# Kernel optimization log

Measured on AMD Instinct MI355X. Metric: run time of the kernel, lower is better.

Reference implementation:

```python
import jax, jax.numpy as jnp
import numpy as np

NUM_TERMS = 8
NUM_CHANNELS = 64
BATCH = 8
NODES = 2048


def setup_inputs() -> dict:
    key = jax.random.key(0)
    kA, kh = jax.random.split(key)
    A = jax.random.normal(kA, (BATCH, NODES, NODES), dtype=jnp.float32)
    # xavier_uniform over (num_terms+1, num_channels)
    fan_in, fan_out = NUM_TERMS + 1, NUM_CHANNELS
    limit = float(np.sqrt(6.0 / (fan_in + fan_out)))
    h = jax.random.uniform(kh, (NUM_TERMS + 1, NUM_CHANNELS), dtype=jnp.float32,
                           minval=-limit, maxval=limit)
    return {"A": A, "h": h}


def reference(A, h):
    # Y[b,n,c] = h[0,c] + sum_{i=1..T} h[i,c] * diag(A^i)[b,n]
    num_terms = h.shape[0] - 1
    diags = []  # each [B, N]: diagonal of A^i
    Ap = A
    for i in range(num_terms):
        if i > 0:
            Ap = jnp.matmul(Ap, A)  # A^(i+1), computed once per power
        diags.append(jnp.diagonal(Ap, axis1=-2, axis2=-1))
    D = jnp.stack(diags, axis=0)  # [T, B, N]
    # fuse per-channel weighted sum of diagonals into one einsum
    out = jnp.einsum("tbn,tc->bnc", D, h[1:])
    out = out + h[0][None, None, :]  # identity term: diag(I) == 1
    return out
```

## Files before the change

### kernel.cpp

```cpp
#include <hip/hip_runtime.h>
#include <hip/hip_bf16.h>

#define NN 2048
#define BB 8
#define NC 64

typedef __bf16 bf16_8 __attribute__((ext_vector_type(8)));
typedef __bf16 bf16_4 __attribute__((ext_vector_type(4)));
typedef float f32x16 __attribute__((ext_vector_type(16)));

__device__ __forceinline__ void gll16(const void* g, void* l) {
  __builtin_amdgcn_global_load_lds((const __attribute__((address_space(1))) void*)g,
                                   (__attribute__((address_space(3))) void*)l,
                                   16, 0, 0);
}

__global__ __launch_bounds__(256)
void k_convert(const float* __restrict__ A, __bf16* __restrict__ Ab, __bf16* __restrict__ At) {
  __shared__ __bf16 tile[64][65];
  int b = blockIdx.z;
  const float* Asrc = A + (size_t)b * NN * NN;
  __bf16* Abd = Ab + (size_t)b * NN * NN;
  __bf16* Atd = At + (size_t)b * NN * NN;
  int r0 = blockIdx.y * 64, c0 = blockIdx.x * 64;
  int row = threadIdx.x >> 4;
  int col4 = (threadIdx.x & 15) * 4;
#pragma unroll
  for (int rr = 0; rr < 64; rr += 16) {
    float4 v = *(const float4*)&Asrc[(size_t)(r0 + row + rr) * NN + c0 + col4];
    bf16_4 hv;
    hv[0] = (__bf16)v.x; hv[1] = (__bf16)v.y; hv[2] = (__bf16)v.z; hv[3] = (__bf16)v.w;
    *(bf16_4*)&Abd[(size_t)(r0 + row + rr) * NN + c0 + col4] = hv;
    tile[row + rr][col4 + 0] = hv[0];
    tile[row + rr][col4 + 1] = hv[1];
    tile[row + rr][col4 + 2] = hv[2];
    tile[row + rr][col4 + 3] = hv[3];
  }
  __syncthreads();
  int row2 = threadIdx.x >> 3;
  int col8 = (threadIdx.x & 7) * 8;
#pragma unroll
  for (int rr = 0; rr < 64; rr += 32) {
    bf16_8 v;
#pragma unroll
    for (int j = 0; j < 8; ++j) v[j] = tile[col8 + j][row2 + rr];
    *(bf16_8*)&Atd[(size_t)(c0 + row2 + rr) * NN + r0 + col8] = v;
  }
}

__global__ __launch_bounds__(256, 2)
void k_gemm_bt(const __bf16* __restrict__ P, const __bf16* __restrict__ Q,
               __bf16* __restrict__ C, __bf16* __restrict__ Ct) {
  __shared__ __align__(16) __bf16 smem[24576];
  __bf16 (*As)[64] = (__bf16(*)[64])smem;
  __bf16 (*Bs)[64] = (__bf16(*)[64])(smem + 16384);
  int b = blockIdx.z;
  const __bf16* Pb = P + (size_t)b * NN * NN;
  const __bf16* Qb = Q + (size_t)b * NN * NN;
  __bf16* Cb = C + (size_t)b * NN * NN;
  int tid = threadIdx.x;
  int wave = tid >> 6;
  int lane = tid & 63;
  int tm = blockIdx.y * 256;
  int tn = blockIdx.x * 128;
  int wm = (wave >> 1) * 128;
  int wn = (wave & 1) * 64;

  int srow = lane >> 3;
  int sc = (lane & 7) ^ srow;
  int arowA = wave * 64;
  int arowB = wave * 32;
  const __bf16* pA = Pb + (size_t)(tm + arowA + srow) * NN + sc * 8;
  const __bf16* pB = Qb + (size_t)(tn + arowB + srow) * NN + sc * 8;

  int am = lane & 31;
  int ah = lane >> 5;

  f32x16 acc[4][2] = {};

  for (int k0 = 0; k0 < NN; k0 += 64) {
#pragma unroll
    for (int g = 0; g < 8; ++g)
      gll16(pA + (size_t)(g * 8) * NN + k0, &As[arowA + g * 8][0]);
#pragma unroll
    for (int g = 0; g < 4; ++g)
      gll16(pB + (size_t)(g * 8) * NN + k0, &Bs[arowB + g * 8][0]);
    __syncthreads();
#pragma unroll
    for (int ks = 0; ks < 4; ++ks) {
      int cch = ks * 2 + ah;
      bf16_8 af[4], bf2[2];
#pragma unroll
      for (int i = 0; i < 4; ++i) {
        int ra = wm + i * 32 + am;
        af[i] = *(const bf16_8*)&As[ra][(cch ^ (ra & 7)) * 8];
      }
#pragma unroll
      for (int i = 0; i < 2; ++i) {
        int rb2 = wn + i * 32 + am;
        bf2[i] = *(const bf16_8*)&Bs[rb2][(cch ^ (rb2 & 7)) * 8];
      }
#pragma unroll
      for (int im = 0; im < 4; ++im)
#pragma unroll
        for (int in = 0; in < 2; ++in)
          acc[im][in] = __builtin_amdgcn_mfma_f32_32x32x16_bf16(af[im], bf2[in], acc[im][in], 0, 0, 0);
    }
    __syncthreads();
  }

  int cc = lane & 31;
  int rq = (lane >> 5) * 4;
#pragma unroll
  for (int im = 0; im < 4; ++im)
#pragma unroll
    for (int in = 0; in < 2; ++in)
#pragma unroll
      for (int reg = 0; reg < 16; ++reg) {
        int row = (reg & 3) + 8 * (reg >> 2) + rq;
        Cb[(size_t)(tm + wm + im * 32 + row) * NN + (tn + wn + in * 32 + cc)] =
            (__bf16)acc[im][in][reg];
      }

  if (Ct != nullptr) {
    __bf16* Ctb = Ct + (size_t)b * NN * NN;
    __bf16 (*Tt)[258] = (__bf16(*)[258])smem;
#pragma unroll
    for (int ch = 0; ch < 2; ++ch) {
      __syncthreads();
      if ((wave & 1) == ch) {
#pragma unroll
        for (int im = 0; im < 4; ++im)
#pragma unroll
          for (int in = 0; in < 2; ++in)
#pragma unroll
            for (int g = 0; g < 4; ++g) {
              bf16_4 v;
#pragma unroll
              for (int r = 0; r < 4; ++r) v[r] = (__bf16)acc[im][in][g * 4 + r];
              *(bf16_4*)&Tt[in * 32 + cc][wm + im * 32 + rq + 8 * g] = v;
            }
      }
      __syncthreads();
#pragma unroll
      for (int p = 0; p < 4; ++p) {
        int trow = p * 16 + (tid >> 4);
        int tcol = (tid & 15) * 16;
        bf16_8 v0 = *(const bf16_8*)&Tt[trow][tcol];
        bf16_8 v1 = *(const bf16_8*)&Tt[trow][tcol + 8];
        size_t gr = (size_t)(tn + ch * 64 + trow) * NN + tm + tcol;
        *(bf16_8*)&Ctb[gr] = v0;
        *(bf16_8*)&Ctb[gr + 8] = v1;
      }
    }
  }
}

__global__ __launch_bounds__(256)
void k_reduce(const float* __restrict__ A, const float* __restrict__ h,
              const __bf16* __restrict__ At, const __bf16* __restrict__ A2,
              const __bf16* __restrict__ A2t, const __bf16* __restrict__ A3t,
              const __bf16* __restrict__ A4, const __bf16* __restrict__ A4t,
              float* __restrict__ out) {
  int b = blockIdx.y;
  int wave = threadIdx.x >> 6, lane = threadIdx.x & 63;
  int n = blockIdx.x * 4 + wave;
  size_t mb = (size_t)b * NN * NN;
  size_t rb = mb + (size_t)n * NN;
  float d5 = 0, d6 = 0, d7 = 0, d8 = 0;
  for (int c = 0; c < NN; c += 512) {
    int k = c + lane * 8;
    bf16_8 va4  = *(const bf16_8*)(A4 + rb + k);
    bf16_8 vat  = *(const bf16_8*)(At + rb + k);
    bf16_8 va2t = *(const bf16_8*)(A2t + rb + k);
    bf16_8 va3t = *(const bf16_8*)(A3t + rb + k);
    bf16_8 va4t = *(const bf16_8*)(A4t + rb + k);
#pragma unroll
    for (int j = 0; j < 8; ++j) {
      float f4 = (float)va4[j];
      d5 += f4 * (float)vat[j];
      d6 += f4 * (float)va2t[j];
      d7 += f4 * (float)va3t[j];
      d8 += f4 * (float)va4t[j];
    }
  }
#pragma unroll
  for (int off = 32; off > 0; off >>= 1) {
    d5 += __shfl_xor(d5, off);
    d6 += __shfl_xor(d6, off);
    d7 += __shfl_xor(d7, off);
    d8 += __shfl_xor(d8, off);
  }
  float d1 = A[mb + (size_t)n * NN + n];
  float d2 = (float)A2[rb + n];
  float d3 = (float)A3t[rb + n];
  float d4 = (float)A4[rb + n];
  float r = h[lane] + h[64 + lane] * d1 + h[128 + lane] * d2 + h[192 + lane] * d3 +
            h[256 + lane] * d4 + h[320 + lane] * d5 + h[384 + lane] * d6 +
            h[448 + lane] * d7 + h[512 + lane] * d8;
  out[((size_t)b * NN + n) * NC + lane] = r;
}

extern "C" void kernel_launch(void* const* d_in, const int* in_sizes, int n_in,
                              void* d_out, int out_size, void* d_ws, size_t ws_size,
                              hipStream_t stream) {
  const float* A = (const float*)d_in[0];
  const float* h = (const float*)d_in[1];
  float* out = (float*)d_out;

  size_t elems = (size_t)BB * NN * NN;
  __bf16* Ab  = (__bf16*)d_ws;
  __bf16* At  = Ab + elems;
  __bf16* A2  = At + elems;
  __bf16* A2t = A2 + elems;
  __bf16* A3t = A2t + elems;
  __bf16* A4  = A3t + elems;
  __bf16* A4t = Ab;

  dim3 bl(256);
  k_convert<<<dim3(32, 32, BB), bl, 0, stream>>>(A, Ab, At);
  k_gemm_bt<<<dim3(16, 8, BB), bl, 0, stream>>>(Ab, At, A2, A2t);
  k_gemm_bt<<<dim3(16, 8, BB), bl, 0, stream>>>(At, A2, A3t, nullptr);
  k_gemm_bt<<<dim3(16, 8, BB), bl, 0, stream>>>(A2, A2t, A4, A4t);
  k_reduce<<<dim3(NN / 4, BB), bl, 0, stream>>>(A, h, At, A2, A2t, A3t, A4, A4t, out);
}
```

Before: 724.9 us.

## Merge the two independent power GEMMs into one launch and raise occupancy

The GEMM body becomes a device function. The A^3 and A^4 products, which depend only on A^2, now run as two jobs selected by blockIdx.z inside a single launch. This removes one kernel boundary and lets the blocks of both GEMMs fill the device together, which should cut tail idle time. Launch bounds go from 2 to 3 blocks per CU to allow more resident blocks, at the risk of register pressure or spills for the 128-float accumulator.

```diff
diff --git a/kernel.cpp b/kernel.cpp
--- a/kernel.cpp
+++ b/kernel.cpp
@@ -48,21 +48,17 @@
   }
 }
 
-__global__ __launch_bounds__(256, 2)
-void k_gemm_bt(const __bf16* __restrict__ P, const __bf16* __restrict__ Q,
-               __bf16* __restrict__ C, __bf16* __restrict__ Ct) {
-  __shared__ __align__(16) __bf16 smem[24576];
+__device__ __forceinline__
+void gemm_body(const __bf16* __restrict__ Pb, const __bf16* __restrict__ Qb,
+               __bf16* __restrict__ Cb, __bf16* __restrict__ Ctb,
+               __bf16* smem, int tmBlk, int tnBlk) {
   __bf16 (*As)[64] = (__bf16(*)[64])smem;
   __bf16 (*Bs)[64] = (__bf16(*)[64])(smem + 16384);
-  int b = blockIdx.z;
-  const __bf16* Pb = P + (size_t)b * NN * NN;
-  const __bf16* Qb = Q + (size_t)b * NN * NN;
-  __bf16* Cb = C + (size_t)b * NN * NN;
   int tid = threadIdx.x;
   int wave = tid >> 6;
   int lane = tid & 63;
-  int tm = blockIdx.y * 256;
-  int tn = blockIdx.x * 128;
+  int tm = tmBlk * 256;
+  int tn = tnBlk * 128;
   int wm = (wave >> 1) * 128;
   int wn = (wave & 1) * 64;
 
@@ -122,8 +118,7 @@
             (__bf16)acc[im][in][reg];
       }
 
-  if (Ct != nullptr) {
-    __bf16* Ctb = Ct + (size_t)b * NN * NN;
+  if (Ctb != nullptr) {
     __bf16 (*Tt)[258] = (__bf16(*)[258])smem;
 #pragma unroll
     for (int ch = 0; ch < 2; ++ch) {
@@ -154,6 +149,28 @@
       }
     }
   }
+}
+
+__global__ __launch_bounds__(256, 3)
+void k_gemm1(const __bf16* __restrict__ Ab, const __bf16* __restrict__ At,
+             __bf16* __restrict__ A2, __bf16* __restrict__ A2t) {
+  __shared__ __align__(16) __bf16 smem[24576];
+  size_t mb = (size_t)blockIdx.z * NN * NN;
+  gemm_body(Ab + mb, At + mb, A2 + mb, A2t + mb, smem, blockIdx.y, blockIdx.x);
+}
+
+__global__ __launch_bounds__(256, 3)
+void k_gemm23(const __bf16* __restrict__ At, const __bf16* __restrict__ A2,
+              const __bf16* __restrict__ A2t,
+              __bf16* __restrict__ A3t, __bf16* __restrict__ A4,
+              __bf16* __restrict__ A4t) {
+  __shared__ __align__(16) __bf16 smem[24576];
+  int job = blockIdx.z >> 3;
+  size_t mb = (size_t)(blockIdx.z & 7) * NN * NN;
+  if (job == 0)
+    gemm_body(At + mb, A2 + mb, A3t + mb, nullptr, smem, blockIdx.y, blockIdx.x);
+  else
+    gemm_body(A2 + mb, A2t + mb, A4 + mb, A4t + mb, smem, blockIdx.y, blockIdx.x);
 }
 
 __global__ __launch_bounds__(256)
@@ -219,8 +236,7 @@
 
   dim3 bl(256);
   k_convert<<<dim3(32, 32, BB), bl, 0, stream>>>(A, Ab, At);
-  k_gemm_bt<<<dim3(16, 8, BB), bl, 0, stream>>>(Ab, At, A2, A2t);
-  k_gemm_bt<<<dim3(16, 8, BB), bl, 0, stream>>>(At, A2, A3t, nullptr);
-  k_gemm_bt<<<dim3(16, 8, BB), bl, 0, stream>>>(A2, A2t, A4, A4t);
+  k_gemm1<<<dim3(16, 8, BB), bl, 0, stream>>>(Ab, At, A2, A2t);
+  k_gemm23<<<dim3(16, 8, 2 * BB), bl, 0, stream>>>(At, A2, A2t, A3t, A4, A4t);
   k_reduce<<<dim3(NN / 4, BB), bl, 0, stream>>>(A, h, At, A2, A2t, A3t, A4, A4t, out);
 }
```

New measurement: 749.5 us. 3.4% more time.
